# Kernel optimization log

Measured on AMD Instinct MI355X. Metric: run time of the kernel, lower is better.

Reference implementation:

```python
import jax, jax.numpy as jnp
import numpy as np

N_NODES = 100000
N_EDGES = 1600000
FEAT = 128
HID = 128
N_GRAPHS = 128


def setup_inputs() -> dict:
    key = jax.random.key(0)
    ks = jax.random.split(key, 20)
    inp = {
        'x': jax.random.normal(ks[0], (N_NODES, FEAT), dtype=jnp.float32),
        'edge_index': jax.random.randint(ks[1], (2, N_EDGES), 0, N_NODES, dtype=jnp.int32),
        'batch': jnp.sort(jax.random.randint(ks[2], (N_NODES,), 0, N_GRAPHS, dtype=jnp.int32)),
        'layer_K': 1,
    }
    # Xavier-uniform weights, zero biases (matches LinearPrune.reset_parameters)
    i = 3
    for l in range(3):
        in_dim = FEAT if l == 0 else HID
        lim1 = float(np.sqrt(6.0 / (in_dim + HID)))
        lim2 = float(np.sqrt(6.0 / (HID + HID)))
        inp[f'W1_l{l}'] = jax.random.uniform(ks[i], (HID, in_dim), jnp.float32, -lim1, lim1); i += 1
        inp[f'b1_l{l}'] = jnp.zeros((HID,), jnp.float32)
        inp[f'W2_l{l}'] = jax.random.uniform(ks[i], (HID, HID), jnp.float32, -lim2, lim2); i += 1
        inp[f'b2_l{l}'] = jnp.zeros((HID,), jnp.float32)
    return inp


def _gin_conv(x, src, dst, W1, b1, W2, b2, k):
    # GINConvPrune.forward with skip=1, eps=0, prune=False
    out = x
    for _ in range(k):  # k = layer_K, static int (deterministic finetune/eval path)
        # propagate: gather neighbor feats then scatter-add at dst nodes
        agg = jax.ops.segment_sum(out[src], dst, num_segments=x.shape[0])
        out = (out + agg) * 0.5
    if k == 0:
        out = jax.ops.segment_sum(x[src], dst, num_segments=x.shape[0])
    out = out + x  # (1 + eps) * x_r with eps = 0
    h = jax.nn.relu(out @ W1.T + b1)
    return h @ W2.T + b2


def reference(x, edge_index, batch, layer_K,
              W1_l0, b1_l0, W2_l0, b2_l0,
              W1_l1, b1_l1, W2_l1, b2_l1,
              W1_l2, b1_l2, W2_l2, b2_l2):
    src, dst = edge_index[0], edge_index[1]
    params = [(W1_l0, b1_l0, W2_l0, b2_l0),
              (W1_l1, b1_l1, W2_l1, b2_l1),
              (W1_l2, b1_l2, W2_l2, b2_l2)]
    k = int(layer_K)
    h = x
    pooled = []
    for (W1, b1, W2, b2) in params:
        h = _gin_conv(h, src, dst, W1, b1, W2, b2, k)
        h = jax.nn.relu(h)  # outer self.act
        pooled.append(jax.ops.segment_sum(h, batch, num_segments=N_GRAPHS))  # global_add_pool
    return jnp.concatenate(pooled, axis=1)  # [G, 3*HID]
```

## Files before the change

### kernel.cpp

```cpp
#include <hip/hip_runtime.h>

#define NN 100000
#define NE 1600000
#define FEAT 128
#define NGRAPH 128
#define BSHIFT 9
#define NB 196
#define NCHUNK 400
#define CHUNK 4000

typedef __attribute__((ext_vector_type(8))) short bf16x8;
typedef __attribute__((ext_vector_type(4))) float f32x4;
typedef __attribute__((ext_vector_type(4))) unsigned u32x4;

union U4 { u32x4 u; bf16x8 v; };

__device__ __forceinline__ unsigned short f2bf(float f) {
    unsigned u = __float_as_uint(f);
    return (unsigned short)((u + 0x7fffu + ((u >> 16) & 1u)) >> 16);
}
__device__ __forceinline__ float bf2f(unsigned short h) {
    return __uint_as_float(((unsigned)h) << 16);
}
__device__ __forceinline__ uint2 unpack2(unsigned p0, unsigned p1) {
    return make_uint2((p0 & 0xffffu) | (p1 << 16), (p0 >> 16) | (p1 & 0xffff0000u));
}
__device__ __forceinline__ void unpack8(u32x4 a, u32x4 b, bf16x8& hv, bf16x8& lv) {
    uint2 r0 = unpack2(a.x, a.y), r1 = unpack2(a.z, a.w);
    uint2 r2 = unpack2(b.x, b.y), r3 = unpack2(b.z, b.w);
    U4 h, l;
    h.u = (u32x4){r0.x, r1.x, r2.x, r3.x};
    l.u = (u32x4){r0.y, r1.y, r2.y, r3.y};
    hv = h.v; lv = l.v;
}

__global__ __launch_bounds__(256)
void wsplit_frag_kernel(const float* __restrict__ W, short* __restrict__ Wf)
{
    int i = blockIdx.x * 256 + threadIdx.x;
    int o = i >> 7, k = i & 127;
    float f = W[i];
    unsigned short h = f2bf(f);
    short lo = (short)f2bf(f - bf2f(h));
    int ct = o >> 4, lr = o & 15, kc = k >> 5, q = (k >> 3) & 3, j = k & 7;
    int idx = (kc * 8 + ct) * 512 + ((q << 4) | lr) * 8 + j;
    Wf[idx] = (short)h;
    Wf[16384 + idx] = lo;
}

__global__ __launch_bounds__(256)
void p1a_count(const int* __restrict__ ei, int* __restrict__ cnt_T)
{
    __shared__ int hist[NB];
    const int b = blockIdx.x, tid = threadIdx.x;
    for (int i = tid; i < NB; i += 256) hist[i] = 0;
    __syncthreads();
    const int e0 = b * CHUNK;
    for (int e = e0 + tid; e < e0 + CHUNK; e += 256)
        atomicAdd(&hist[ei[NE + e] >> BSHIFT], 1);
    __syncthreads();
    for (int k = tid; k < NB; k += 256) cnt_T[k * NCHUNK + b] = hist[k];
}

__global__ __launch_bounds__(1024)
void scan1_kernel(const int* __restrict__ in, int* __restrict__ out,
                  int* __restrict__ bsum, int n)
{
    __shared__ int sh[1024];
    const int tid = threadIdx.x;
    const int gid = blockIdx.x * 1024 + tid;
    int v = (gid < n) ? in[gid] : 0;
    sh[tid] = v;
    __syncthreads();
    #pragma unroll
    for (int d = 1; d < 1024; d <<= 1) {
        int t = (tid >= d) ? sh[tid - d] : 0;
        __syncthreads();
        sh[tid] += t;
        __syncthreads();
    }
    if (gid < n) out[gid] = sh[tid] - v;
    if (tid == 1023) bsum[blockIdx.x] = sh[1023];
}

__global__ __launch_bounds__(128)
void scan2_kernel(int* __restrict__ bsum, int nb)
{
    __shared__ int sh[128];
    const int tid = threadIdx.x;
    int v = (tid < nb) ? bsum[tid] : 0;
    sh[tid] = v;
    __syncthreads();
    #pragma unroll
    for (int d = 1; d < 128; d <<= 1) {
        int t = (tid >= d) ? sh[tid - d] : 0;
        __syncthreads();
        sh[tid] += t;
        __syncthreads();
    }
    if (tid < nb) bsum[tid] = sh[tid] - v;
}

__global__ __launch_bounds__(1024)
void scan3g_kernel(int* __restrict__ arr, const int* __restrict__ bsum, int n)
{
    const int gid = blockIdx.x * 1024 + threadIdx.x;
    if (gid < n) arr[gid] += bsum[blockIdx.x];
}

__global__ __launch_bounds__(256)
void p1b_scatter(const int* __restrict__ ei, const int* __restrict__ offs_T,
                 int2* __restrict__ ebuf)
{
    __shared__ int cur[NB];
    const int b = blockIdx.x, tid = threadIdx.x;
    for (int i = tid; i < NB; i += 256) cur[i] = offs_T[i * NCHUNK + b];
    __syncthreads();
    const int e0 = b * CHUNK;
    for (int e = e0 + tid; e < e0 + CHUNK; e += 256) {
        int s = ei[e], d = ei[NE + e];
        int pos = atomicAdd(&cur[d >> BSHIFT], 1);
        ebuf[pos] = make_int2(s, d);
    }
}

__global__ __launch_bounds__(512)
void p2_csr(const int2* __restrict__ ebuf, const int* __restrict__ offs_T,
            int* __restrict__ off, int* __restrict__ csr)
{
    __shared__ int degc[512];
    __shared__ int sh[512];
    const int k = blockIdx.x, tid = threadIdx.x;
    const int base = k << BSHIFT;
    const int bs = offs_T[k * NCHUNK];
    const int be = (k == NB - 1) ? NE : offs_T[(k + 1) * NCHUNK];
    degc[tid] = 0;
    __syncthreads();
    for (int e = bs + tid; e < be; e += 512)
        atomicAdd(&degc[ebuf[e].y - base], 1);
    __syncthreads();
    int v = degc[tid];
    sh[tid] = v;
    __syncthreads();
    #pragma unroll
    for (int d = 1; d < 512; d <<= 1) {
        int t = (tid >= d) ? sh[tid - d] : 0;
        __syncthreads();
        sh[tid] += t;
        __syncthreads();
    }
    const int excl = bs + sh[tid] - v;
    const int n = base + tid;
    if (n <= NN) off[n] = excl;
    degc[tid] = excl;
    __syncthreads();
    for (int e = bs + tid; e < be; e += 512) {
        int2 p = ebuf[e];
        int slot = atomicAdd(&degc[p.y - base], 1);
        csr[slot] = p.x;
    }
}

__global__ __launch_bounds__(256)
void aggregate_pack_kernel(const float* __restrict__ h, const int* __restrict__ off,
                           const int* __restrict__ csr, unsigned* __restrict__ xP, int nn)
{
    const int node = blockIdx.x * 4 + (threadIdx.x >> 6);
    if (node >= nn) return;
    const int lane = threadIdx.x & 63;
    const int s = off[node], e = off[node + 1];
    float2 acc = make_float2(0.f, 0.f);
    for (int base = s; base < e; base += 64) {
        const int cnt = min(64, e - base);
        int src_l = (base + lane < e) ? csr[base + lane] : 0;
        for (int jb = 0; jb < cnt; jb += 16) {
            float2 v[16];
            #pragma unroll
            for (int q = 0; q < 16; ++q) {
                int sq = __shfl(src_l, (jb + q) & 63);
                v[q] = reinterpret_cast<const float2*>(h + (size_t)sq * FEAT)[lane];
            }
            #pragma unroll
            for (int q = 0; q < 16; ++q) {
                if (jb + q < cnt) { acc.x += v[q].x; acc.y += v[q].y; }
            }
        }
    }
    float2 hv = reinterpret_cast<const float2*>(h + (size_t)node * FEAT)[lane];
    float ox = (hv.x + acc.x) * 0.5f + hv.x;
    float oy = (hv.y + acc.y) * 0.5f + hv.y;
    unsigned short hx = f2bf(ox), hy = f2bf(oy);
    unsigned wx = (unsigned)hx | ((unsigned)f2bf(ox - bf2f(hx)) << 16);
    unsigned wy = (unsigned)hy | ((unsigned)f2bf(oy - bf2f(hy)) << 16);
    uint2 pw = make_uint2(wx, wy);
    *reinterpret_cast<uint2*>(&xP[(size_t)node * FEAT + lane * 2]) = pw;
}

__global__ __launch_bounds__(512, 4)
void gemm_mfma5_kernel(const unsigned* __restrict__ aP, const short* __restrict__ Wf,
                       const float* __restrict__ bias, float* __restrict__ outF,
                       unsigned* __restrict__ outP, int n_nodes)
{
    __shared__ short wlds[32768];
    const int tid = threadIdx.x;
    const int lane = tid & 63;
    const int w = tid >> 6;
    const int lr = lane & 15;
    const int lq = lane >> 4;
    const int row0 = blockIdx.x * 256 + w * 32;

    {
        const bf16x8* src = reinterpret_cast<const bf16x8*>(Wf);
        bf16x8* dst = reinterpret_cast<bf16x8*>(wlds);
        #pragma unroll
        for (int it = 0; it < 8; ++it)
            dst[it * 512 + tid] = src[it * 512 + tid];
    }

    const int n0 = row0 + lr;
    const int n1 = row0 + 16 + lr;
    const bool v0 = (n0 < n_nodes), v1 = (n1 < n_nodes);
    const size_t rb0 = (size_t)n0 * FEAT + lq * 8;
    const size_t rb1 = (size_t)n1 * FEAT + lq * 8;
    u32x4 zz = {};

    u32x4 pa0a = v0 ? *reinterpret_cast<const u32x4*>(&aP[rb0])     : zz;
    u32x4 pa0b = v0 ? *reinterpret_cast<const u32x4*>(&aP[rb0 + 4]) : zz;
    u32x4 pa1a = v1 ? *reinterpret_cast<const u32x4*>(&aP[rb1])     : zz;
    u32x4 pa1b = v1 ? *reinterpret_cast<const u32x4*>(&aP[rb1 + 4]) : zz;
    __syncthreads();

    f32x4 acc[2][8] = {};
    bf16x8 ah0, al0, ah1, al1;
    unpack8(pa0a, pa0b, ah0, al0);
    unpack8(pa1a, pa1b, ah1, al1);

    #pragma unroll
    for (int kc = 0; kc < 4; ++kc) {
        u32x4 n0a = zz, n0b = zz, n1a = zz, n1b = zz;
        if (kc < 3) {
            const int ko = (kc + 1) * 32;
            n0a = v0 ? *reinterpret_cast<const u32x4*>(&aP[rb0 + ko])     : zz;
            n0b = v0 ? *reinterpret_cast<const u32x4*>(&aP[rb0 + ko + 4]) : zz;
            n1a = v1 ? *reinterpret_cast<const u32x4*>(&aP[rb1 + ko])     : zz;
            n1b = v1 ? *reinterpret_cast<const u32x4*>(&aP[rb1 + ko + 4]) : zz;
        }
        #pragma unroll
        for (int ct = 0; ct < 8; ++ct) {
            const int ra = (kc * 8 + ct) * 512 + lane * 8;
            bf16x8 bh = *reinterpret_cast<const bf16x8*>(&wlds[ra]);
            bf16x8 bl = *reinterpret_cast<const bf16x8*>(&wlds[16384 + ra]);
            acc[0][ct] = __builtin_amdgcn_mfma_f32_16x16x32_bf16(bh, ah0, acc[0][ct], 0, 0, 0);
            acc[0][ct] = __builtin_amdgcn_mfma_f32_16x16x32_bf16(bh, al0, acc[0][ct], 0, 0, 0);
            acc[0][ct] = __builtin_amdgcn_mfma_f32_16x16x32_bf16(bl, ah0, acc[0][ct], 0, 0, 0);
            acc[1][ct] = __builtin_amdgcn_mfma_f32_16x16x32_bf16(bh, ah1, acc[1][ct], 0, 0, 0);
            acc[1][ct] = __builtin_amdgcn_mfma_f32_16x16x32_bf16(bh, al1, acc[1][ct], 0, 0, 0);
            acc[1][ct] = __builtin_amdgcn_mfma_f32_16x16x32_bf16(bl, ah1, acc[1][ct], 0, 0, 0);
        }
        if (kc < 3) {
            unpack8(n0a, n0b, ah0, al0);
            unpack8(n1a, n1b, ah1, al1);
        }
    }

    #pragma unroll
    for (int nt = 0; nt < 2; ++nt) {
        const int n = row0 + nt * 16 + lr;
        if (n >= n_nodes) continue;
        #pragma unroll
        for (int ct = 0; ct < 8; ++ct) {
            const int c0 = ct * 16 + lq * 4;
            float4 bv = *reinterpret_cast<const float4*>(&bias[c0]);
            f32x4 a = acc[nt][ct];
            float e0 = fmaxf(a[0] + bv.x, 0.f);
            float e1 = fmaxf(a[1] + bv.y, 0.f);
            float e2 = fmaxf(a[2] + bv.z, 0.f);
            float e3 = fmaxf(a[3] + bv.w, 0.f);
            if (outF) {
                float4 o = make_float4(e0, e1, e2, e3);
                *reinterpret_cast<float4*>(&outF[(size_t)n * FEAT + c0]) = o;
            } else {
                unsigned short h0 = f2bf(e0), h1 = f2bf(e1), h2 = f2bf(e2), h3 = f2bf(e3);
                u32x4 pw;
                pw.x = (unsigned)h0 | ((unsigned)f2bf(e0 - bf2f(h0)) << 16);
                pw.y = (unsigned)h1 | ((unsigned)f2bf(e1 - bf2f(h1)) << 16);
                pw.z = (unsigned)h2 | ((unsigned)f2bf(e2 - bf2f(h2)) << 16);
                pw.w = (unsigned)h3 | ((unsigned)f2bf(e3 - bf2f(h3)) << 16);
                *reinterpret_cast<u32x4*>(&outP[(size_t)n * FEAT + c0]) = pw;
            }
        }
    }
}

__global__ __launch_bounds__(512)
void pool_kernel(const float* __restrict__ y, const int* __restrict__ batch,
                 float* __restrict__ out, int n_nodes, int layer)
{
    const int g = blockIdx.x;
    int lo = 0, hi = n_nodes;
    while (lo < hi) { int mid = (lo + hi) >> 1; if (batch[mid] < g) lo = mid + 1; else hi = mid; }
    const int start = lo;
    hi = n_nodes;
    while (lo < hi) { int mid = (lo + hi) >> 1; if (batch[mid] < g + 1) lo = mid + 1; else hi = mid; }
    const int end = lo;

    const int tid = threadIdx.x;
    const int f = tid & 127;
    const int q = tid >> 7;
    float sum = 0.f;
    for (int n = start + q; n < end; n += 4)
        sum += y[(size_t)n * FEAT + f];

    __shared__ float red[512];
    red[tid] = sum;
    __syncthreads();
    if (tid < 128)
        out[g * (3 * FEAT) + layer * FEAT + tid]
            = red[tid] + red[tid + 128] + red[tid + 256] + red[tid + 384];
}

__global__ __launch_bounds__(256)
void scatter_kernel(const float* __restrict__ h, const int* __restrict__ ei,
                    float* __restrict__ agg, int n_edges)
{
    int e = blockIdx.x * 4 + (threadIdx.x >> 6);
    if (e >= n_edges) return;
    int lane = threadIdx.x & 63;
    int s = ei[e];
    int d = ei[n_edges + e];
    float2 v = reinterpret_cast<const float2*>(h + (size_t)s * FEAT)[lane];
    float* ap = agg + (size_t)d * FEAT + lane * 2;
    atomicAdd(ap, v.x);
    atomicAdd(ap + 1, v.y);
}

__global__ __launch_bounds__(256)
void combine_kernel(const float* __restrict__ h, float* __restrict__ agg_xeff, size_t n4)
{
    size_t i = (size_t)blockIdx.x * 256 + threadIdx.x;
    if (i >= n4) return;
    float4 a = reinterpret_cast<const float4*>(h)[i];
    float4 g = reinterpret_cast<float4*>(agg_xeff)[i];
    float4 o;
    o.x = (a.x + g.x) * 0.5f + a.x;
    o.y = (a.y + g.y) * 0.5f + a.y;
    o.z = (a.z + g.z) * 0.5f + a.z;
    o.w = (a.w + g.w) * 0.5f + a.w;
    reinterpret_cast<float4*>(agg_xeff)[i] = o;
}

__global__ __launch_bounds__(256, 2)
void gemm_relu_kernel(const float* __restrict__ A, const float* __restrict__ W,
                      const float* __restrict__ bias, float* __restrict__ out, int n_nodes)
{
    __shared__ float xt[64][128];
    __shared__ float wt[64][128];
    const int tid = threadIdx.x;
    const int row0 = blockIdx.x * 128;
    const int r  = tid >> 1;
    const int ks = (tid & 1) << 5;
    const int tn = (tid >> 4) << 3;
    const int to = (tid & 15) << 3;
    float acc[8][8] = {};

    for (int c = 0; c < 2; ++c) {
        const int k0 = c * 64;
        {
            const float4* wrow = reinterpret_cast<const float4*>(W + r * FEAT + k0 + ks);
            #pragma unroll
            for (int i = 0; i < 8; ++i) {
                float4 w4 = wrow[i];
                int kk = ks + i * 4;
                wt[kk + 0][r] = w4.x; wt[kk + 1][r] = w4.y;
                wt[kk + 2][r] = w4.z; wt[kk + 3][r] = w4.w;
            }
        }
        {
            const int n = row0 + r;
            if (n < n_nodes) {
                const float4* ar = reinterpret_cast<const float4*>(A + (size_t)n * FEAT + k0 + ks);
                #pragma unroll
                for (int i = 0; i < 8; ++i) {
                    float4 a4 = ar[i];
                    int kk = ks + i * 4;
                    xt[kk + 0][r] = a4.x; xt[kk + 1][r] = a4.y;
                    xt[kk + 2][r] = a4.z; xt[kk + 3][r] = a4.w;
                }
            } else {
                #pragma unroll
                for (int i = 0; i < 8; ++i) {
                    int kk = ks + i * 4;
                    xt[kk + 0][r] = 0.f; xt[kk + 1][r] = 0.f;
                    xt[kk + 2][r] = 0.f; xt[kk + 3][r] = 0.f;
                }
            }
        }
        __syncthreads();
        #pragma unroll 4
        for (int k = 0; k < 64; ++k) {
            float4 x0 = *reinterpret_cast<const float4*>(&xt[k][tn]);
            float4 x1 = *reinterpret_cast<const float4*>(&xt[k][tn + 4]);
            float4 w0 = *reinterpret_cast<const float4*>(&wt[k][to]);
            float4 w1 = *reinterpret_cast<const float4*>(&wt[k][to + 4]);
            float xv[8] = {x0.x, x0.y, x0.z, x0.w, x1.x, x1.y, x1.z, x1.w};
            float wv[8] = {w0.x, w0.y, w0.z, w0.w, w1.x, w1.y, w1.z, w1.w};
            #pragma unroll
            for (int i = 0; i < 8; ++i)
                #pragma unroll
                for (int j = 0; j < 8; ++j)
                    acc[i][j] = fmaf(xv[i], wv[j], acc[i][j]);
        }
        __syncthreads();
    }

    float bv[8];
    #pragma unroll
    for (int j = 0; j < 8; ++j) bv[j] = bias[to + j];
    #pragma unroll
    for (int i = 0; i < 8; ++i) {
        int n = row0 + tn + i;
        if (n >= n_nodes) break;
        float4 o0, o1;
        o0.x = fmaxf(acc[i][0] + bv[0], 0.f);
        o0.y = fmaxf(acc[i][1] + bv[1], 0.f);
        o0.z = fmaxf(acc[i][2] + bv[2], 0.f);
        o0.w = fmaxf(acc[i][3] + bv[3], 0.f);
        o1.x = fmaxf(acc[i][4] + bv[4], 0.f);
        o1.y = fmaxf(acc[i][5] + bv[5], 0.f);
        o1.z = fmaxf(acc[i][6] + bv[6], 0.f);
        o1.w = fmaxf(acc[i][7] + bv[7], 0.f);
        float* op = out + (size_t)n * FEAT + to;
        *reinterpret_cast<float4*>(op) = o0;
        *reinterpret_cast<float4*>(op + 4) = o1;
    }
}

extern "C" void kernel_launch(void* const* d_in, const int* in_sizes, int n_in,
                              void* d_out, int out_size, void* d_ws, size_t ws_size,
                              hipStream_t stream)
{
    const float* x     = (const float*)d_in[0];
    const int*   ei    = (const int*)d_in[1];
    const int*   batch = (const int*)d_in[2];
    const float* W1[3] = {(const float*)d_in[4], (const float*)d_in[8],  (const float*)d_in[12]};
    const float* b1[3] = {(const float*)d_in[5], (const float*)d_in[9],  (const float*)d_in[13]};
    const float* W2[3] = {(const float*)d_in[6], (const float*)d_in[10], (const float*)d_in[14]};
    const float* b2[3] = {(const float*)d_in[7], (const float*)d_in[11], (const float*)d_in[15]};

    const size_t nf = (size_t)NN * FEAT;
    float* outp = (float*)d_out;
    const int gemm_grid = (NN + 255) / 256;
    const int M = NB * NCHUNK;
    const int scanM_blocks = (M + 1023) / 1024;
    const int WN = FEAT * FEAT;

    const size_t need_full = 3 * nf * 4 + (size_t)(NN + 1 + NE) * 4 + (size_t)12 * WN * 2;

    if (ws_size >= need_full) {
        unsigned* xeffP = (unsigned*)d_ws;
        unsigned* h1P   = xeffP + nf;
        float* bufC     = (float*)(h1P + nf);
        int* off        = (int*)(bufC + nf);
        int* csr        = off + (NN + 1);
        short* wbase    = (short*)(csr + NE);
        short* wf[6];
        for (int i = 0; i < 6; ++i) wf[i] = wbase + (size_t)i * 2 * WN;
        int* cnt_T  = (int*)xeffP;
        int* offs_T = cnt_T + M;
        int* bsum   = offs_T + M;
        int2* ebuf  = (int2*)h1P;

        const float* Ws[6] = {W1[0], W2[0], W1[1], W2[1], W1[2], W2[2]};
        for (int i = 0; i < 6; ++i)
            wsplit_frag_kernel<<<WN / 256, 256, 0, stream>>>(Ws[i], wf[i]);

        p1a_count<<<NCHUNK, 256, 0, stream>>>(ei, cnt_T);
        scan1_kernel<<<scanM_blocks, 1024, 0, stream>>>(cnt_T, offs_T, bsum, M);
        scan2_kernel<<<1, 128, 0, stream>>>(bsum, scanM_blocks);
        scan3g_kernel<<<scanM_blocks, 1024, 0, stream>>>(offs_T, bsum, M);
        p1b_scatter<<<NCHUNK, 256, 0, stream>>>(ei, offs_T, ebuf);
        p2_csr<<<NB, 512, 0, stream>>>(ebuf, offs_T, off, csr);

        const float* h = x;
        for (int l = 0; l < 3; ++l) {
            aggregate_pack_kernel<<<(NN + 3) / 4, 256, 0, stream>>>(h, off, csr, xeffP, NN);
            gemm_mfma5_kernel<<<gemm_grid, 512, 0, stream>>>(xeffP, wf[2 * l], b1[l],
                                                             nullptr, h1P, NN);
            gemm_mfma5_kernel<<<gemm_grid, 512, 0, stream>>>(h1P, wf[2 * l + 1], b2[l],
                                                             bufC, nullptr, NN);
            pool_kernel<<<NGRAPH, 512, 0, stream>>>(bufC, batch, outp, NN, l);
            h = bufC;
        }
    } else if (ws_size >= 3 * nf * 4) {
        float* bufA = (float*)d_ws;
        float* bufB = bufA + nf;
        float* bufC = bufB + nf;
        const int gg = (NN + 127) / 128;
        const float* h = x;
        for (int l = 0; l < 3; ++l) {
            hipMemsetAsync(bufA, 0, nf * 4, stream);
            scatter_kernel<<<(NE + 3) / 4, 256, 0, stream>>>(h, ei, bufA, NE);
            combine_kernel<<<(int)((nf / 4 + 255) / 256), 256, 0, stream>>>(h, bufA, nf / 4);
            gemm_relu_kernel<<<gg, 256, 0, stream>>>(bufA, W1[l], b1[l], bufB, NN);
            gemm_relu_kernel<<<gg, 256, 0, stream>>>(bufB, W2[l], b2[l], bufC, NN);
            pool_kernel<<<NGRAPH, 512, 0, stream>>>(bufC, batch, outp, NN, l);
            h = bufC;
        }
    }
}
```

Measured before the change: 721.8 us.

## Fuse both GIN MLP GEMMs into one kernel keeping hidden activations in registers

The two per-layer GEMM launches become a single kernel. It computes the first linear layer plus ReLU, keeps the split-bf16 hidden activations in registers, and reshuffles them with wave shuffles into MFMA operand layout for the second GEMM. This removes the write and re-read of the 100000x128 packed intermediate buffer and one launch per layer. In exchange, each block now covers 128 rows instead of 256, so the weight loads into LDS are amortized over fewer rows and each block loads LDS twice. Register pressure and shuffle overhead also go up.

```diff
diff --git a/kernel.cpp b/kernel.cpp
--- a/kernel.cpp
+++ b/kernel.cpp
@@ -21,6 +21,10 @@
 }
 __device__ __forceinline__ float bf2f(unsigned short h) {
     return __uint_as_float(((unsigned)h) << 16);
+}
+__device__ __forceinline__ unsigned packbf(float f) {
+    unsigned short h = f2bf(f);
+    return (unsigned)h | ((unsigned)f2bf(f - bf2f(h)) << 16);
 }
 __device__ __forceinline__ uint2 unpack2(unsigned p0, unsigned p1) {
     return make_uint2((p0 & 0xffffu) | (p1 << 16), (p0 >> 16) | (p1 & 0xffff0000u));
@@ -189,17 +193,14 @@
     float2 hv = reinterpret_cast<const float2*>(h + (size_t)node * FEAT)[lane];
     float ox = (hv.x + acc.x) * 0.5f + hv.x;
     float oy = (hv.y + acc.y) * 0.5f + hv.y;
-    unsigned short hx = f2bf(ox), hy = f2bf(oy);
-    unsigned wx = (unsigned)hx | ((unsigned)f2bf(ox - bf2f(hx)) << 16);
-    unsigned wy = (unsigned)hy | ((unsigned)f2bf(oy - bf2f(hy)) << 16);
-    uint2 pw = make_uint2(wx, wy);
+    uint2 pw = make_uint2(packbf(ox), packbf(oy));
     *reinterpret_cast<uint2*>(&xP[(size_t)node * FEAT + lane * 2]) = pw;
 }
 
 __global__ __launch_bounds__(512, 4)
-void gemm_mfma5_kernel(const unsigned* __restrict__ aP, const short* __restrict__ Wf,
-                       const float* __restrict__ bias, float* __restrict__ outF,
-                       unsigned* __restrict__ outP, int n_nodes)
+void layer_fused_kernel(const unsigned* __restrict__ aP, const short* __restrict__ Wf1,
+                        const short* __restrict__ Wf2, const float* __restrict__ b1,
+                        const float* __restrict__ b2, float* __restrict__ outC, int n_nodes)
 {
     __shared__ short wlds[32768];
     const int tid = threadIdx.x;
@@ -207,87 +208,109 @@
     const int w = tid >> 6;
     const int lr = lane & 15;
     const int lq = lane >> 4;
-    const int row0 = blockIdx.x * 256 + w * 32;
+    const int n0 = blockIdx.x * 128 + w * 16 + lr;
+    const bool v0 = (n0 < n_nodes);
+    const size_t rb0 = (size_t)n0 * FEAT + lq * 8;
+    u32x4 zz = {};
 
     {
-        const bf16x8* src = reinterpret_cast<const bf16x8*>(Wf);
+        const bf16x8* src = reinterpret_cast<const bf16x8*>(Wf1);
         bf16x8* dst = reinterpret_cast<bf16x8*>(wlds);
         #pragma unroll
         for (int it = 0; it < 8; ++it)
             dst[it * 512 + tid] = src[it * 512 + tid];
     }
-
-    const int n0 = row0 + lr;
-    const int n1 = row0 + 16 + lr;
-    const bool v0 = (n0 < n_nodes), v1 = (n1 < n_nodes);
-    const size_t rb0 = (size_t)n0 * FEAT + lq * 8;
-    const size_t rb1 = (size_t)n1 * FEAT + lq * 8;
-    u32x4 zz = {};
-
-    u32x4 pa0a = v0 ? *reinterpret_cast<const u32x4*>(&aP[rb0])     : zz;
-    u32x4 pa0b = v0 ? *reinterpret_cast<const u32x4*>(&aP[rb0 + 4]) : zz;
-    u32x4 pa1a = v1 ? *reinterpret_cast<const u32x4*>(&aP[rb1])     : zz;
-    u32x4 pa1b = v1 ? *reinterpret_cast<const u32x4*>(&aP[rb1 + 4]) : zz;
-    __syncthreads();
-
-    f32x4 acc[2][8] = {};
-    bf16x8 ah0, al0, ah1, al1;
-    unpack8(pa0a, pa0b, ah0, al0);
-    unpack8(pa1a, pa1b, ah1, al1);
-
+    u32x4 paa = v0 ? *reinterpret_cast<const u32x4*>(&aP[rb0])     : zz;
+    u32x4 pab = v0 ? *reinterpret_cast<const u32x4*>(&aP[rb0 + 4]) : zz;
+    __syncthreads();
+
+    f32x4 acc[8] = {};
+    bf16x8 ah, al;
+    unpack8(paa, pab, ah, al);
     #pragma unroll
     for (int kc = 0; kc < 4; ++kc) {
-        u32x4 n0a = zz, n0b = zz, n1a = zz, n1b = zz;
+        u32x4 na = zz, nb = zz;
         if (kc < 3) {
             const int ko = (kc + 1) * 32;
-            n0a = v0 ? *reinterpret_cast<const u32x4*>(&aP[rb0 + ko])     : zz;
-            n0b = v0 ? *reinterpret_cast<const u32x4*>(&aP[rb0 + ko + 4]) : zz;
-            n1a = v1 ? *reinterpret_cast<const u32x4*>(&aP[rb1 + ko])     : zz;
-            n1b = v1 ? *reinterpret_cast<const u32x4*>(&aP[rb1 + ko + 4]) : zz;
+            na = v0 ? *reinterpret_cast<const u32x4*>(&aP[rb0 + ko])     : zz;
+            nb = v0 ? *reinterpret_cast<const u32x4*>(&aP[rb0 + ko + 4]) : zz;
         }
         #pragma unroll
         for (int ct = 0; ct < 8; ++ct) {
             const int ra = (kc * 8 + ct) * 512 + lane * 8;
             bf16x8 bh = *reinterpret_cast<const bf16x8*>(&wlds[ra]);
             bf16x8 bl = *reinterpret_cast<const bf16x8*>(&wlds[16384 + ra]);
-            acc[0][ct] = __builtin_amdgcn_mfma_f32_16x16x32_bf16(bh, ah0, acc[0][ct], 0, 0, 0);
-            acc[0][ct] = __builtin_amdgcn_mfma_f32_16x16x32_bf16(bh, al0, acc[0][ct], 0, 0, 0);
-            acc[0][ct] = __builtin_amdgcn_mfma_f32_16x16x32_bf16(bl, ah0, acc[0][ct], 0, 0, 0);
-            acc[1][ct] = __builtin_amdgcn_mfma_f32_16x16x32_bf16(bh, ah1, acc[1][ct], 0, 0, 0);
-            acc[1][ct] = __builtin_amdgcn_mfma_f32_16x16x32_bf16(bh, al1, acc[1][ct], 0, 0, 0);
-            acc[1][ct] = __builtin_amdgcn_mfma_f32_16x16x32_bf16(bl, ah1, acc[1][ct], 0, 0, 0);
-        }
-        if (kc < 3) {
-            unpack8(n0a, n0b, ah0, al0);
-            unpack8(n1a, n1b, ah1, al1);
-        }
-    }
-
-    #pragma unroll
-    for (int nt = 0; nt < 2; ++nt) {
-        const int n = row0 + nt * 16 + lr;
-        if (n >= n_nodes) continue;
+            acc[ct] = __builtin_amdgcn_mfma_f32_16x16x32_bf16(bh, ah, acc[ct], 0, 0, 0);
+            acc[ct] = __builtin_amdgcn_mfma_f32_16x16x32_bf16(bh, al, acc[ct], 0, 0, 0);
+            acc[ct] = __builtin_amdgcn_mfma_f32_16x16x32_bf16(bl, ah, acc[ct], 0, 0, 0);
+        }
+        if (kc < 3) unpack8(na, nb, ah, al);
+    }
+
+    unsigned h1p[32];
+    #pragma unroll
+    for (int ct = 0; ct < 8; ++ct) {
+        const int c0 = ct * 16 + lq * 4;
+        float4 bv = *reinterpret_cast<const float4*>(&b1[c0]);
+        h1p[ct * 4 + 0] = packbf(fmaxf(acc[ct][0] + bv.x, 0.f));
+        h1p[ct * 4 + 1] = packbf(fmaxf(acc[ct][1] + bv.y, 0.f));
+        h1p[ct * 4 + 2] = packbf(fmaxf(acc[ct][2] + bv.z, 0.f));
+        h1p[ct * 4 + 3] = packbf(fmaxf(acc[ct][3] + bv.w, 0.f));
+    }
+
+    __syncthreads();
+    {
+        const bf16x8* src = reinterpret_cast<const bf16x8*>(Wf2);
+        bf16x8* dst = reinterpret_cast<bf16x8*>(wlds);
+        #pragma unroll
+        for (int it = 0; it < 8; ++it)
+            dst[it * 512 + tid] = src[it * 512 + tid];
+    }
+    __syncthreads();
+
+    f32x4 acc2[8] = {};
+    const int aown = (lq & 1) * 2;
+    const bool hi_t = (lq & 2) != 0;
+    #pragma unroll
+    for (int kc = 0; kc < 4; ++kc) {
+        unsigned pd[8];
+        #pragma unroll
+        for (int m = 0; m < 4; ++m) {
+            unsigned vA = h1p[(2 * kc) * 4 + m];
+            unsigned vB = h1p[(2 * kc + 1) * 4 + m];
+            unsigned sA0 = __shfl(vA, lr + 16 * aown);
+            unsigned sB0 = __shfl(vB, lr + 16 * aown);
+            unsigned sA1 = __shfl(vA, lr + 16 * (aown + 1));
+            unsigned sB1 = __shfl(vB, lr + 16 * (aown + 1));
+            pd[m]     = hi_t ? sB0 : sA0;
+            pd[4 + m] = hi_t ? sB1 : sA1;
+        }
+        u32x4 qa = {pd[0], pd[1], pd[2], pd[3]};
+        u32x4 qb = {pd[4], pd[5], pd[6], pd[7]};
+        bf16x8 hh, hl;
+        unpack8(qa, qb, hh, hl);
+        #pragma unroll
+        for (int ct = 0; ct < 8; ++ct) {
+            const int ra = (kc * 8 + ct) * 512 + lane * 8;
+            bf16x8 bh = *reinterpret_cast<const bf16x8*>(&wlds[ra]);
+            bf16x8 bl = *reinterpret_cast<const bf16x8*>(&wlds[16384 + ra]);
+            acc2[ct] = __builtin_amdgcn_mfma_f32_16x16x32_bf16(bh, hh, acc2[ct], 0, 0, 0);
+            acc2[ct] = __builtin_amdgcn_mfma_f32_16x16x32_bf16(bh, hl, acc2[ct], 0, 0, 0);
+            acc2[ct] = __builtin_amdgcn_mfma_f32_16x16x32_bf16(bl, hh, acc2[ct], 0, 0, 0);
+        }
+    }
+
+    if (v0) {
         #pragma unroll
         for (int ct = 0; ct < 8; ++ct) {
             const int c0 = ct * 16 + lq * 4;
-            float4 bv = *reinterpret_cast<const float4*>(&bias[c0]);
-            f32x4 a = acc[nt][ct];
-            float e0 = fmaxf(a[0] + bv.x, 0.f);
-            float e1 = fmaxf(a[1] + bv.y, 0.f);
-            float e2 = fmaxf(a[2] + bv.z, 0.f);
-            float e3 = fmaxf(a[3] + bv.w, 0.f);
-            if (outF) {
-                float4 o = make_float4(e0, e1, e2, e3);
-                *reinterpret_cast<float4*>(&outF[(size_t)n * FEAT + c0]) = o;
-            } else {
-                unsigned short h0 = f2bf(e0), h1 = f2bf(e1), h2 = f2bf(e2), h3 = f2bf(e3);
-                u32x4 pw;
-                pw.x = (unsigned)h0 | ((unsigned)f2bf(e0 - bf2f(h0)) << 16);
-                pw.y = (unsigned)h1 | ((unsigned)f2bf(e1 - bf2f(h1)) << 16);
-                pw.z = (unsigned)h2 | ((unsigned)f2bf(e2 - bf2f(h2)) << 16);
-                pw.w = (unsigned)h3 | ((unsigned)f2bf(e3 - bf2f(h3)) << 16);
-                *reinterpret_cast<u32x4*>(&outP[(size_t)n * FEAT + c0]) = pw;
-            }
+            float4 bv = *reinterpret_cast<const float4*>(&b2[c0]);
+            float4 o;
+            o.x = fmaxf(acc2[ct][0] + bv.x, 0.f);
+            o.y = fmaxf(acc2[ct][1] + bv.y, 0.f);
+            o.z = fmaxf(acc2[ct][2] + bv.z, 0.f);
+            o.w = fmaxf(acc2[ct][3] + bv.w, 0.f);
+            *reinterpret_cast<float4*>(&outC[(size_t)n0 * FEAT + c0]) = o;
         }
     }
 }
@@ -449,17 +472,16 @@
 
     const size_t nf = (size_t)NN * FEAT;
     float* outp = (float*)d_out;
-    const int gemm_grid = (NN + 255) / 256;
+    const int fused_grid = (NN + 127) / 128;
     const int M = NB * NCHUNK;
     const int scanM_blocks = (M + 1023) / 1024;
     const int WN = FEAT * FEAT;
 
-    const size_t need_full = 3 * nf * 4 + (size_t)(NN + 1 + NE) * 4 + (size_t)12 * WN * 2;
+    const size_t need_full = 2 * nf * 4 + (size_t)(NN + 1 + NE) * 4 + (size_t)12 * WN * 2;
 
     if (ws_size >= need_full) {
         unsigned* xeffP = (unsigned*)d_ws;
-        unsigned* h1P   = xeffP + nf;
-        float* bufC     = (float*)(h1P + nf);
+        float* bufC     = (float*)(xeffP + nf);
         int* off        = (int*)(bufC + nf);
         int* csr        = off + (NN + 1);
         short* wbase    = (short*)(csr + NE);
@@ -468,7 +490,7 @@
         int* cnt_T  = (int*)xeffP;
         int* offs_T = cnt_T + M;
         int* bsum   = offs_T + M;
-        int2* ebuf  = (int2*)h1P;
+        int2* ebuf  = (int2*)bufC;
 
         const float* Ws[6] = {W1[0], W2[0], W1[1], W2[1], W1[2], W2[2]};
         for (int i = 0; i < 6; ++i)
@@ -484,10 +506,8 @@
         const float* h = x;
         for (int l = 0; l < 3; ++l) {
             aggregate_pack_kernel<<<(NN + 3) / 4, 256, 0, stream>>>(h, off, csr, xeffP, NN);
-            gemm_mfma5_kernel<<<gemm_grid, 512, 0, stream>>>(xeffP, wf[2 * l], b1[l],
-                                                             nullptr, h1P, NN);
-            gemm_mfma5_kernel<<<gemm_grid, 512, 0, stream>>>(h1P, wf[2 * l + 1], b2[l],
-                                                             bufC, nullptr, NN);
+            layer_fused_kernel<<<fused_grid, 512, 0, stream>>>(xeffP, wf[2 * l], wf[2 * l + 1],
+                                                               b1[l], b2[l], bufC, NN);
             pool_kernel<<<NGRAPH, 512, 0, stream>>>(bufC, batch, outp, NN, l);
             h = bufC;
         }
```

Result: faster. 692.2 us (median of 2 runs) (-4.1%).
